# Kernel optimization log

Measured on AMD Instinct MI355X. Metric: run time of the kernel, lower is better.

Reference implementation:

```python
import jax, jax.numpy as jnp
import numpy as np
from jax import lax

TF_ALPHA = 0.125


def _teacher_force(z, x, alpha):
    # z: (B, dz), x: (B, dx); force first dx dims of z where x is not NaN
    dx = x.shape[-1]
    head = z[:, :dx]
    forced = jnp.where(jnp.isnan(x), head, alpha * x + (1.0 - alpha) * head)
    return jnp.concatenate([forced, z[:, dx:]], axis=-1)


def setup_inputs() -> dict:
    key = jax.random.key(0)
    ks = jax.random.split(key, 8)
    B, T, dx, dz, dh, ds = 256, 1024, 64, 128, 512, 16
    X = jax.random.normal(ks[0], (B, T, dx), dtype=jnp.float32)
    inputs = jax.random.normal(ks[1], (B, T, ds), dtype=jnp.float32)
    # A in (0, 0.9) for stable linear part; small weight scales to avoid blowup over T steps
    A = jax.random.uniform(ks[2], (B, dz), dtype=jnp.float32) * 0.9
    W1 = jax.random.normal(ks[3], (B, dz, dh), dtype=jnp.float32) * (0.5 / np.sqrt(dh))
    W2 = jax.random.normal(ks[4], (B, dh, dz), dtype=jnp.float32) * (0.5 / np.sqrt(dz))
    h1 = jax.random.normal(ks[5], (B, dz), dtype=jnp.float32) * 0.1
    h2 = jax.random.normal(ks[6], (B, dh), dtype=jnp.float32) * 0.1
    C = jax.random.normal(ks[7], (B, dz, ds), dtype=jnp.float32) * (0.5 / np.sqrt(ds))
    return {"X": X, "inputs": inputs, "A": A, "W1": W1, "W2": W2,
            "h1": h1, "h2": h2, "C": C}


def _plrnn_forward(X, inputs, A, W1, W2, h1, h2, C):
    B, T, dx = X.shape
    dz = A.shape[-1]
    # z0 = zeros teacher-forced with alpha=1 from X[:, 0]
    z0 = jnp.zeros((B, dz), dtype=X.dtype)
    z0 = _teacher_force(z0, X[:, 0], alpha=1.0)

    Xt = jnp.transpose(X, (1, 0, 2))        # (T, B, dx)
    St = jnp.transpose(inputs, (1, 0, 2))   # (T, B, ds)

    def step(z, xs):
        x_t, s_t = xs
        zf = _teacher_force(z, x_t, TF_ALPHA)
        pre = jnp.einsum('bhz,bz->bh', W2, zf) + h2          # (B, dh)
        z_new = (A * zf
                 + jnp.einsum('bzh,bh->bz', W1, jax.nn.relu(pre))
                 + h1
                 + jnp.einsum('bzs,bs->bz', C, s_t))
        return z_new, z_new

    _, Z = lax.scan(step, z0, (Xt, St))      # Z: (T, B, dz)
    Z = jnp.transpose(Z, (1, 0, 2))          # (B, T, dz)
    return Z[:, :, :dx]                      # dim_x_proj == 0 path


def reference(X, inputs, A, W1, W2, h1, h2, C):
    return _plrnn_forward(X, inputs, A, W1, W2, h1, h2, C)
```

## Files before the change

kernel.cpp:

```cpp
#include <hip/hip_runtime.h>
#include <math.h>


#define NB 256
#define T  1024
#define DX 64
#define DZ 128
#define DH 512
#define DS 16
#define CHUNK 128

typedef _Float16 half8 __attribute__((ext_vector_type(8)));
typedef _Float16 v4h   __attribute__((ext_vector_type(4)));
typedef float    f32x4 __attribute__((ext_vector_type(4)));

__device__ __forceinline__ half8 cvt8(const float* __restrict__ src) {
  const float4 a = *reinterpret_cast<const float4*>(src);
  const float4 c = *reinterpret_cast<const float4*>(src + 4);
  half8 h;
  h[0] = (_Float16)a.x; h[1] = (_Float16)a.y; h[2] = (_Float16)a.z; h[3] = (_Float16)a.w;
  h[4] = (_Float16)c.x; h[5] = (_Float16)c.y; h[6] = (_Float16)c.z; h[7] = (_Float16)c.w;
  return h;
}

__device__ __forceinline__ f32x4 sel4(int c, f32x4 a, f32x4 b) {
  f32x4 r;
  r[0] = c ? a[0] : b[0];  r[1] = c ? a[1] : b[1];
  r[2] = c ? a[2] : b[2];  r[3] = c ? a[3] : b[3];
  return r;
}

template <int CTRL>
__device__ __forceinline__ f32x4 dpp_xor_add(f32x4 v) {
  f32x4 r;
  #pragma unroll
  for (int j = 0; j < 4; ++j) {
    const int t = __builtin_amdgcn_update_dpp(0, __float_as_int(v[j]), CTRL, 0xF, 0xF, true);
    r[j] = v[j] + __int_as_float(t);
  }
  return r;
}

__device__ __forceinline__ f32x4 swz_xor4_add(f32x4 v) {
  f32x4 r;
  #pragma unroll
  for (int j = 0; j < 4; ++j) {
    const int t = __builtin_amdgcn_ds_swizzle(__float_as_int(v[j]), 0x101F);
    r[j] = v[j] + __int_as_float(t);
  }
  return r;
}

__global__ __launch_bounds__(512, 2) void plrnn_kernel(
    const float* __restrict__ X, const float* __restrict__ S,
    const float* __restrict__ A, const float* __restrict__ W1,
    const float* __restrict__ W2, const float* __restrict__ h1,
    const float* __restrict__ h2, const float* __restrict__ C,
    float* __restrict__ out)
{
  __shared__ __align__(16) _Float16 zf_h[DZ];
  __shared__ __align__(16) _Float16 rt[544];
  __shared__ __align__(16) float    part[8][132];
  __shared__ __align__(16) float    Xc[CHUNK][DX];
  __shared__ __align__(16) float    Sc[CHUNK][DS];
  __shared__ __align__(16) float    outc[CHUNK][DX];

  const int b   = blockIdx.x;
  const int tid = threadIdx.x;
  const int w   = tid >> 6;
  const int l   = tid & 63;
  const int g   = l >> 4;
  const int r15 = l & 15;
  const int zb  = (l >> 3) & 3;

  {
    #pragma unroll
    for (int k = 0; k < 4; ++k) {
      const int flat = k * 2048 + tid * 4;
      int srow = 1 + (flat >> 6);
      if (srow > T - 1) srow = T - 1;
      const float4 v = *reinterpret_cast<const float4*>(X + ((size_t)b * T + srow) * DX + (flat & 63));
      *reinterpret_cast<float4*>(&((float*)Xc)[flat]) = v;
    }
    const int flat = tid * 4;
    const float4 v = *reinterpret_cast<const float4*>(S + ((size_t)b * T) * DS + flat);
    *reinterpret_cast<float4*>(&((float*)Sc)[flat]) = v;
  }

  if (tid < 16) rt[528 + tid] = (tid == 0) ? (_Float16)1.0f : (_Float16)0.0f;

  half8 w2f[4][4];
  #pragma unroll
  for (int mt = 0; mt < 4; ++mt)
    #pragma unroll
    for (int kt = 0; kt < 4; ++kt)
      w2f[mt][kt] = cvt8(W2 + ((size_t)b * DH + 64 * w + 16 * mt + r15) * DZ + 32 * kt + 8 * g);

  half8 w1f[8][2];
  #pragma unroll
  for (int mt = 0; mt < 8; ++mt)
    #pragma unroll
    for (int kt = 0; kt < 2; ++kt)
      w1f[mt][kt] = cvt8(W1 + ((size_t)b * DZ + 16 * mt + r15) * DH + 64 * w + 32 * kt + 8 * g);

  half8 w1ft[8];
  #pragma unroll
  for (int mt = 0; mt < 8; ++mt)
    #pragma unroll
    for (int e = 0; e < 8; ++e) w1ft[mt][e] = (_Float16)0.0f;
  if (w == 0) {
    #pragma unroll
    for (int mt = 0; mt < 8; ++mt) {
      const int row = 16 * mt + r15;
      if (g == 0)      w1ft[mt] = cvt8(C + ((size_t)b * DZ + row) * DS + 0);
      else if (g == 1) w1ft[mt] = cvt8(C + ((size_t)b * DZ + row) * DS + 8);
      else if (g == 2) w1ft[mt][0] = (_Float16)h1[(size_t)b * DZ + row];
    }
  }

  f32x4 h2v[4];
  #pragma unroll
  for (int mt = 0; mt < 4; ++mt)
    h2v[mt] = *reinterpret_cast<const f32x4*>(h2 + (size_t)b * DH + 64 * w + 16 * mt + 4 * g);

  const f32x4 Areg = *reinterpret_cast<const f32x4*>(A + (size_t)b * DZ + 16 * w + 4 * zb);
  f32x4 zfcur = {0.f, 0.f, 0.f, 0.f};
  if (w < 4) {
    const f32x4 x0 = *reinterpret_cast<const f32x4*>(X + ((size_t)b * T) * DX + 16 * w + 4 * zb);
    #pragma unroll
    for (int j = 0; j < 4; ++j) zfcur[j] = (x0[j] != x0[j]) ? 0.f : x0[j];
  }
  if (l < 32 && (l & 7) == 0) {
    v4h zp;
    #pragma unroll
    for (int j = 0; j < 4; ++j) zp[j] = (_Float16)zfcur[j];
    *reinterpret_cast<v4h*>(&zf_h[16 * w + 4 * zb]) = zp;
  }
  __syncthreads();

  const f32x4 zero4 = {0.f, 0.f, 0.f, 0.f};

  for (int t = 0; t < T; ++t) {
    if ((t & (CHUNK - 1)) == 0 && t) {
      const int c0 = t - CHUNK;
      #pragma unroll
      for (int k = 0; k < 4; ++k) {
        const int flat = k * 2048 + tid * 4;
        const float4 v = *reinterpret_cast<const float4*>(&((float*)outc)[flat]);
        *reinterpret_cast<float4*>(out + ((size_t)b * T + c0) * DX + flat) = v;
      }
      #pragma unroll
      for (int k = 0; k < 4; ++k) {
        const int flat = k * 2048 + tid * 4;
        int srow = t + 1 + (flat >> 6);
        if (srow > T - 1) srow = T - 1;
        const float4 v = *reinterpret_cast<const float4*>(X + ((size_t)b * T + srow) * DX + (flat & 63));
        *reinterpret_cast<float4*>(&((float*)Xc)[flat]) = v;
      }
      const int flat = tid * 4;
      const float4 v = *reinterpret_cast<const float4*>(S + ((size_t)b * T + t) * DS + flat);
      *reinterpret_cast<float4*>(&((float*)Sc)[flat]) = v;
      __syncthreads();
    }
    const int tc = t & (CHUNK - 1);

    if (w == 0 && l < 4) {
      const f32x4 sv = *reinterpret_cast<const f32x4*>(&Sc[tc][4 * l]);
      v4h sp;
      #pragma unroll
      for (int j = 0; j < 4; ++j) sp[j] = (_Float16)sv[j];
      *reinterpret_cast<v4h*>(&rt[512 + 4 * l]) = sp;
    }

    half8 bz[4];
    #pragma unroll
    for (int kt = 0; kt < 4; ++kt)
      bz[kt] = *reinterpret_cast<const half8*>(zf_h + 32 * kt + 8 * g);

    f32x4 acc1[4];
    #pragma unroll
    for (int mt = 0; mt < 4; ++mt)
      acc1[mt] = __builtin_amdgcn_mfma_f32_16x16x32_f16(w2f[mt][0], bz[0], h2v[mt], 0, 0, 0);
    #pragma unroll
    for (int kt = 1; kt < 4; ++kt)
      #pragma unroll
      for (int mt = 0; mt < 4; ++mt)
        acc1[mt] = __builtin_amdgcn_mfma_f32_16x16x32_f16(w2f[mt][kt], bz[kt], acc1[mt], 0, 0, 0);

    {
      const f32x4 lo = sel4(r15 & 1, acc1[1], acc1[0]);
      const f32x4 hi = sel4(r15 & 1, acc1[3], acc1[2]);
      const f32x4 sv = sel4(r15 & 2, hi, lo);
      if (r15 < 4) {
        v4h p;
        #pragma unroll
        for (int j = 0; j < 4; ++j) p[j] = (_Float16)fmaxf(sv[j], 0.f);
        *reinterpret_cast<v4h*>(&rt[64 * w + 16 * r15 + 4 * g]) = p;
      }
    }

    half8 br[2];
    #pragma unroll
    for (int kt = 0; kt < 2; ++kt)
      br[kt] = *reinterpret_cast<const half8*>(rt + 64 * w + 32 * kt + 8 * g);

    f32x4 acc2[8];
    #pragma unroll
    for (int mt = 0; mt < 8; ++mt)
      acc2[mt] = __builtin_amdgcn_mfma_f32_16x16x32_f16(w1f[mt][0], br[0], zero4, 0, 0, 0);
    #pragma unroll
    for (int mt = 0; mt < 8; ++mt)
      acc2[mt] = __builtin_amdgcn_mfma_f32_16x16x32_f16(w1f[mt][1], br[1], acc2[mt], 0, 0, 0);
    if (w == 0) {
      const half8 brt = *reinterpret_cast<const half8*>(rt + 512 + 8 * g);
      #pragma unroll
      for (int mt = 0; mt < 8; ++mt)
        acc2[mt] = __builtin_amdgcn_mfma_f32_16x16x32_f16(w1ft[mt], brt, acc2[mt], 0, 0, 0);
    }

    {
      const f32x4 s01 = sel4(r15 & 1, acc2[1], acc2[0]);
      const f32x4 s23 = sel4(r15 & 1, acc2[3], acc2[2]);
      const f32x4 s45 = sel4(r15 & 1, acc2[5], acc2[4]);
      const f32x4 s67 = sel4(r15 & 1, acc2[7], acc2[6]);
      const f32x4 a03 = sel4(r15 & 2, s23, s01);
      const f32x4 a47 = sel4(r15 & 2, s67, s45);
      const f32x4 sv  = sel4(r15 & 4, a47, a03);
      if (r15 < 8)
        *reinterpret_cast<f32x4*>(&part[w][16 * r15 + 4 * g]) = sv;
    }
    __syncthreads();

    f32x4 u = *reinterpret_cast<const f32x4*>(&part[l & 7][16 * w + 4 * zb]);
    u = dpp_xor_add<0xB1>(u);
    u = dpp_xor_add<0x4E>(u);
    u = swz_xor4_add(u);

    f32x4 zn, zfn;
    #pragma unroll
    for (int j = 0; j < 4; ++j) zn[j] = Areg[j] * zfcur[j] + u[j];
    zfn = zn;
    if (w < 4) {
      const f32x4 xv = *reinterpret_cast<const f32x4*>(&Xc[tc][16 * w + 4 * zb]);
      #pragma unroll
      for (int j = 0; j < 4; ++j)
        zfn[j] = (xv[j] != xv[j]) ? zn[j] : (0.125f * xv[j] + 0.875f * zn[j]);
      if (l < 32 && (l & 7) == 0)
        *reinterpret_cast<f32x4*>(&outc[tc][16 * w + 4 * zb]) = zn;
    }
    zfcur = zfn;
    if (l < 32 && (l & 7) == 0) {
      v4h zp;
      #pragma unroll
      for (int j = 0; j < 4; ++j) zp[j] = (_Float16)zfn[j];
      *reinterpret_cast<v4h*>(&zf_h[16 * w + 4 * zb]) = zp;
    }
    __syncthreads();
  }

  {
    const int c0 = T - CHUNK;
    #pragma unroll
    for (int k = 0; k < 4; ++k) {
      const int flat = k * 2048 + tid * 4;
      const float4 v = *reinterpret_cast<const float4*>(&((float*)outc)[flat]);
      *reinterpret_cast<float4*>(out + ((size_t)b * T + c0) * DX + flat) = v;
    }
  }
}

extern "C" void kernel_launch(void* const* d_in, const int* in_sizes, int n_in,
                              void* d_out, int out_size, void* d_ws, size_t ws_size,
                              hipStream_t stream) {
  const float* X  = (const float*)d_in[0];
  const float* S  = (const float*)d_in[1];
  const float* A  = (const float*)d_in[2];
  const float* W1 = (const float*)d_in[3];
  const float* W2 = (const float*)d_in[4];
  const float* h1 = (const float*)d_in[5];
  const float* h2 = (const float*)d_in[6];
  const float* C  = (const float*)d_in[7];
  float* out = (float*)d_out;
  plrnn_kernel<<<dim3(NB), dim3(512), 0, stream>>>(X, S, A, W1, W2, h1, h2, C, out);
}
```

Before: 1.087 ms.

## Spread input-projection MFMA across waves and simplify per-step reduction path

The C/h1 tail MFMA, which only wave 0 ran as 8 extra MFMAs, is split so each wave computes one 16-row tile and folds it into the accumulator init of its matching output tile. The select-based lane compaction of MFMA outputs is replaced by a single lane per row group writing all tiles directly. The cross-wave reduction now reads two partials per lane, which removes the ds_swizzle stage, and the partial buffer stride is padded. Staging of the next step's inputs into rt is moved into the previous iteration's tail to drop work from the serial critical path. The trade-off is more LDS store traffic from fewer lanes.

```diff
diff --git a/kernel.cpp b/kernel.cpp
--- a/kernel.cpp
+++ b/kernel.cpp
@@ -9,6 +9,7 @@
 #define DH 512
 #define DS 16
 #define CHUNK 128
+#define PSTR 136
 
 typedef _Float16 half8 __attribute__((ext_vector_type(8)));
 typedef _Float16 v4h   __attribute__((ext_vector_type(4)));
@@ -23,29 +24,12 @@
   return h;
 }
 
-__device__ __forceinline__ f32x4 sel4(int c, f32x4 a, f32x4 b) {
-  f32x4 r;
-  r[0] = c ? a[0] : b[0];  r[1] = c ? a[1] : b[1];
-  r[2] = c ? a[2] : b[2];  r[3] = c ? a[3] : b[3];
-  return r;
-}
-
 template <int CTRL>
 __device__ __forceinline__ f32x4 dpp_xor_add(f32x4 v) {
   f32x4 r;
   #pragma unroll
   for (int j = 0; j < 4; ++j) {
     const int t = __builtin_amdgcn_update_dpp(0, __float_as_int(v[j]), CTRL, 0xF, 0xF, true);
-    r[j] = v[j] + __int_as_float(t);
-  }
-  return r;
-}
-
-__device__ __forceinline__ f32x4 swz_xor4_add(f32x4 v) {
-  f32x4 r;
-  #pragma unroll
-  for (int j = 0; j < 4; ++j) {
-    const int t = __builtin_amdgcn_ds_swizzle(__float_as_int(v[j]), 0x101F);
     r[j] = v[j] + __int_as_float(t);
   }
   return r;
@@ -60,7 +44,7 @@
 {
   __shared__ __align__(16) _Float16 zf_h[DZ];
   __shared__ __align__(16) _Float16 rt[544];
-  __shared__ __align__(16) float    part[8][132];
+  __shared__ __align__(16) float    part[8][PSTR];
   __shared__ __align__(16) float    Xc[CHUNK][DX];
   __shared__ __align__(16) float    Sc[CHUNK][DS];
   __shared__ __align__(16) float    outc[CHUNK][DX];
@@ -71,7 +55,8 @@
   const int l   = tid & 63;
   const int g   = l >> 4;
   const int r15 = l & 15;
-  const int zb  = (l >> 3) & 3;
+  const int zb  = (l >> 2) & 3;
+  const int a4  = l & 3;
 
   {
     #pragma unroll
@@ -87,7 +72,10 @@
     *reinterpret_cast<float4*>(&((float*)Sc)[flat]) = v;
   }
 
-  if (tid < 16) rt[528 + tid] = (tid == 0) ? (_Float16)1.0f : (_Float16)0.0f;
+  if (tid < 16) {
+    rt[528 + tid] = (tid == 0) ? (_Float16)1.0f : (_Float16)0.0f;
+    rt[512 + tid] = (_Float16)S[((size_t)b * T) * DS + tid];
+  }
 
   half8 w2f[4][4];
   #pragma unroll
@@ -103,19 +91,14 @@
     for (int kt = 0; kt < 2; ++kt)
       w1f[mt][kt] = cvt8(W1 + ((size_t)b * DZ + 16 * mt + r15) * DH + 64 * w + 32 * kt + 8 * g);
 
-  half8 w1ft[8];
-  #pragma unroll
-  for (int mt = 0; mt < 8; ++mt)
-    #pragma unroll
-    for (int e = 0; e < 8; ++e) w1ft[mt][e] = (_Float16)0.0f;
-  if (w == 0) {
-    #pragma unroll
-    for (int mt = 0; mt < 8; ++mt) {
-      const int row = 16 * mt + r15;
-      if (g == 0)      w1ft[mt] = cvt8(C + ((size_t)b * DZ + row) * DS + 0);
-      else if (g == 1) w1ft[mt] = cvt8(C + ((size_t)b * DZ + row) * DS + 8);
-      else if (g == 2) w1ft[mt][0] = (_Float16)h1[(size_t)b * DZ + row];
-    }
+  half8 w1ft;
+  #pragma unroll
+  for (int e = 0; e < 8; ++e) w1ft[e] = (_Float16)0.0f;
+  {
+    const int row = 16 * w + r15;
+    if (g == 0)      w1ft = cvt8(C + ((size_t)b * DZ + row) * DS + 0);
+    else if (g == 1) w1ft = cvt8(C + ((size_t)b * DZ + row) * DS + 8);
+    else if (g == 2) w1ft[0] = (_Float16)h1[(size_t)b * DZ + row];
   }
 
   f32x4 h2v[4];
@@ -130,7 +113,7 @@
     #pragma unroll
     for (int j = 0; j < 4; ++j) zfcur[j] = (x0[j] != x0[j]) ? 0.f : x0[j];
   }
-  if (l < 32 && (l & 7) == 0) {
+  if (l < 16 && a4 == 0) {
     v4h zp;
     #pragma unroll
     for (int j = 0; j < 4; ++j) zp[j] = (_Float16)zfcur[j];
@@ -157,20 +140,15 @@
         const float4 v = *reinterpret_cast<const float4*>(X + ((size_t)b * T + srow) * DX + (flat & 63));
         *reinterpret_cast<float4*>(&((float*)Xc)[flat]) = v;
       }
-      const int flat = tid * 4;
-      const float4 v = *reinterpret_cast<const float4*>(S + ((size_t)b * T + t) * DS + flat);
-      *reinterpret_cast<float4*>(&((float*)Sc)[flat]) = v;
+      {
+        const int flat = tid * 4;
+        const float4 v = *reinterpret_cast<const float4*>(S + ((size_t)b * T + t) * DS + flat);
+        *reinterpret_cast<float4*>(&((float*)Sc)[flat]) = v;
+      }
+      if (tid < 16) rt[512 + tid] = (_Float16)S[((size_t)b * T + t) * DS + tid];
       __syncthreads();
     }
     const int tc = t & (CHUNK - 1);
-
-    if (w == 0 && l < 4) {
-      const f32x4 sv = *reinterpret_cast<const f32x4*>(&Sc[tc][4 * l]);
-      v4h sp;
-      #pragma unroll
-      for (int j = 0; j < 4; ++j) sp[j] = (_Float16)sv[j];
-      *reinterpret_cast<v4h*>(&rt[512 + 4 * l]) = sp;
-    }
 
     half8 bz[4];
     #pragma unroll
@@ -187,54 +165,45 @@
       for (int mt = 0; mt < 4; ++mt)
         acc1[mt] = __builtin_amdgcn_mfma_f32_16x16x32_f16(w2f[mt][kt], bz[kt], acc1[mt], 0, 0, 0);
 
-    {
-      const f32x4 lo = sel4(r15 & 1, acc1[1], acc1[0]);
-      const f32x4 hi = sel4(r15 & 1, acc1[3], acc1[2]);
-      const f32x4 sv = sel4(r15 & 2, hi, lo);
-      if (r15 < 4) {
+    if (r15 == 0) {
+      #pragma unroll
+      for (int mt = 0; mt < 4; ++mt) {
         v4h p;
-        #pragma unroll
-        for (int j = 0; j < 4; ++j) p[j] = (_Float16)fmaxf(sv[j], 0.f);
-        *reinterpret_cast<v4h*>(&rt[64 * w + 16 * r15 + 4 * g]) = p;
-      }
-    }
-
-    half8 br[2];
-    #pragma unroll
-    for (int kt = 0; kt < 2; ++kt)
-      br[kt] = *reinterpret_cast<const half8*>(rt + 64 * w + 32 * kt + 8 * g);
+        p[0] = (_Float16)fmaxf(acc1[mt][0], 0.f);
+        p[1] = (_Float16)fmaxf(acc1[mt][1], 0.f);
+        p[2] = (_Float16)fmaxf(acc1[mt][2], 0.f);
+        p[3] = (_Float16)fmaxf(acc1[mt][3], 0.f);
+        *reinterpret_cast<v4h*>(&rt[64 * w + 16 * mt + 4 * g]) = p;
+      }
+    }
+
+    const half8 br0 = *reinterpret_cast<const half8*>(rt + 64 * w + 8 * g);
+    const half8 br1 = *reinterpret_cast<const half8*>(rt + 64 * w + 32 + 8 * g);
+    const half8 brt = *reinterpret_cast<const half8*>(rt + 512 + 8 * g);
+
+    const f32x4 tailv = __builtin_amdgcn_mfma_f32_16x16x32_f16(w1ft, brt, zero4, 0, 0, 0);
 
     f32x4 acc2[8];
     #pragma unroll
     for (int mt = 0; mt < 8; ++mt)
-      acc2[mt] = __builtin_amdgcn_mfma_f32_16x16x32_f16(w1f[mt][0], br[0], zero4, 0, 0, 0);
+      acc2[mt] = __builtin_amdgcn_mfma_f32_16x16x32_f16(w1f[mt][0], br0,
+                                                        (mt == w) ? tailv : zero4, 0, 0, 0);
     #pragma unroll
     for (int mt = 0; mt < 8; ++mt)
-      acc2[mt] = __builtin_amdgcn_mfma_f32_16x16x32_f16(w1f[mt][1], br[1], acc2[mt], 0, 0, 0);
-    if (w == 0) {
-      const half8 brt = *reinterpret_cast<const half8*>(rt + 512 + 8 * g);
+      acc2[mt] = __builtin_amdgcn_mfma_f32_16x16x32_f16(w1f[mt][1], br1, acc2[mt], 0, 0, 0);
+
+    if (r15 == 0) {
       #pragma unroll
       for (int mt = 0; mt < 8; ++mt)
-        acc2[mt] = __builtin_amdgcn_mfma_f32_16x16x32_f16(w1ft[mt], brt, acc2[mt], 0, 0, 0);
-    }
-
-    {
-      const f32x4 s01 = sel4(r15 & 1, acc2[1], acc2[0]);
-      const f32x4 s23 = sel4(r15 & 1, acc2[3], acc2[2]);
-      const f32x4 s45 = sel4(r15 & 1, acc2[5], acc2[4]);
-      const f32x4 s67 = sel4(r15 & 1, acc2[7], acc2[6]);
-      const f32x4 a03 = sel4(r15 & 2, s23, s01);
-      const f32x4 a47 = sel4(r15 & 2, s67, s45);
-      const f32x4 sv  = sel4(r15 & 4, a47, a03);
-      if (r15 < 8)
-        *reinterpret_cast<f32x4*>(&part[w][16 * r15 + 4 * g]) = sv;
+        *reinterpret_cast<f32x4*>(&part[w][16 * mt + 4 * g]) = acc2[mt];
     }
     __syncthreads();
 
-    f32x4 u = *reinterpret_cast<const f32x4*>(&part[l & 7][16 * w + 4 * zb]);
+    const f32x4 u1 = *reinterpret_cast<const f32x4*>(&part[a4][16 * w + 4 * zb]);
+    const f32x4 u2 = *reinterpret_cast<const f32x4*>(&part[4 + a4][16 * w + 4 * zb]);
+    f32x4 u = u1 + u2;
     u = dpp_xor_add<0xB1>(u);
     u = dpp_xor_add<0x4E>(u);
-    u = swz_xor4_add(u);
 
     f32x4 zn, zfn;
     #pragma unroll
@@ -245,15 +214,22 @@
       #pragma unroll
       for (int j = 0; j < 4; ++j)
         zfn[j] = (xv[j] != xv[j]) ? zn[j] : (0.125f * xv[j] + 0.875f * zn[j]);
-      if (l < 32 && (l & 7) == 0)
+      if (l < 16 && a4 == 0)
         *reinterpret_cast<f32x4*>(&outc[tc][16 * w + 4 * zb]) = zn;
     }
     zfcur = zfn;
-    if (l < 32 && (l & 7) == 0) {
+    if (l < 16 && a4 == 0) {
       v4h zp;
       #pragma unroll
       for (int j = 0; j < 4; ++j) zp[j] = (_Float16)zfn[j];
       *reinterpret_cast<v4h*>(&zf_h[16 * w + 4 * zb]) = zp;
+    }
+    if (w == 7 && l < 4 && ((t + 1) & (CHUNK - 1)) != 0) {
+      const f32x4 sv = *reinterpret_cast<const f32x4*>(&Sc[(t + 1) & (CHUNK - 1)][4 * l]);
+      v4h sp;
+      #pragma unroll
+      for (int j = 0; j < 4; ++j) sp[j] = (_Float16)sv[j];
+      *reinterpret_cast<v4h*>(&rt[512 + 4 * l]) = sp;
     }
     __syncthreads();
   }
```

New measurement: 1.336 ms. 1.23x slower.
